# Kernel tuning notes

Measured on AMD Instinct MI355X. Metric: run time of the kernel, lower is better.

Reference implementation:

```python
import jax, jax.numpy as jnp
import numpy as np

B, S, D_MODEL, NUM_HEADS, DFF = 4, 2048, 256, 8, 1024
DEPTH = D_MODEL // NUM_HEADS
EPS = 1e-6
LENGTH_SCALE = 1.0


def setup_inputs() -> dict:
    key = jax.random.key(0)
    ks = jax.random.split(key, 18)
    n = lambda k, shp, s=0.05: (jax.random.normal(k, shp, dtype=jnp.float32) * s)
    return {
        "x": jax.random.normal(ks[0], (B, S, D_MODEL), dtype=jnp.float32),
        "wq_w": n(ks[1], (D_MODEL, D_MODEL)), "wq_b": jnp.zeros((D_MODEL,), jnp.float32),
        "wk_w": n(ks[2], (D_MODEL, D_MODEL)), "wk_b": jnp.zeros((D_MODEL,), jnp.float32),
        "wv_w": n(ks[3], (D_MODEL, D_MODEL)), "wv_b": jnp.zeros((D_MODEL,), jnp.float32),
        "wo_w": n(ks[4], (D_MODEL, D_MODEL)), "wo_b": jnp.zeros((D_MODEL,), jnp.float32),
        "ffn1_w": n(ks[5], (D_MODEL, DFF)), "ffn1_b": jnp.zeros((DFF,), jnp.float32),
        "ffn2_w": n(ks[6], (DFF, D_MODEL)), "ffn2_b": jnp.zeros((D_MODEL,), jnp.float32),
        "ln1_g": jnp.ones((D_MODEL,), jnp.float32), "ln1_b": jnp.zeros((D_MODEL,), jnp.float32),
        "ln2_g": jnp.ones((D_MODEL,), jnp.float32), "ln2_b": jnp.zeros((D_MODEL,), jnp.float32),
    }


def _layernorm(x, g, b):
    mu = jnp.mean(x, axis=-1, keepdims=True)
    var = jnp.mean(jnp.square(x - mu), axis=-1, keepdims=True)
    return (x - mu) * jax.lax.rsqrt(var + EPS) * g + b


def _split_heads(t):
    # [B,S,D_MODEL] -> [B,H,S,depth]
    return t.reshape(B, S, NUM_HEADS, DEPTH).transpose(0, 2, 1, 3)


def _encoder_layer(x, wq_w, wq_b, wk_w, wk_b, wv_w, wv_b, wo_w, wo_b,
                   ffn1_w, ffn1_b, ffn2_w, ffn2_b, ln1_g, ln1_b, ln2_g, ln2_b):
    q = _split_heads(x @ wq_w + wq_b)
    k = _split_heads(x @ wk_w + wk_b)
    v = _split_heads(x @ wv_w + wv_b)
    # pairwise squared distances: ||q||^2 - 2 q.k + ||k||^2 -> [B,H,S,S]
    q2 = jnp.sum(q * q, axis=-1)  # [B,H,S]
    k2 = jnp.sum(k * k, axis=-1)  # [B,H,S]
    dists = q2[..., :, None] - 2.0 * jnp.einsum("bhqd,bhkd->bhqk", q, k) + k2[..., None, :]
    # exponentiated-quadratic kernel, then softmax over keys (mask=None)
    attn = jax.nn.softmax(jnp.exp(-0.5 * dists / (LENGTH_SCALE ** 2)), axis=-1)
    out = jnp.einsum("bhqk,bhkd->bhqd", attn, v)  # [B,H,S,depth]
    out = out.transpose(0, 2, 1, 3).reshape(B, S, D_MODEL)
    attn_out = out @ wo_w + wo_b
    # dropout is identity (training=False)
    out1 = _layernorm(x + attn_out, ln1_g, ln1_b)
    ffn = jax.nn.relu(out1 @ ffn1_w + ffn1_b) @ ffn2_w + ffn2_b
    return _layernorm(out1 + ffn, ln2_g, ln2_b)


def reference(x, wq_w, wq_b, wk_w, wk_b, wv_w, wv_b, wo_w, wo_b,
              ffn1_w, ffn1_b, ffn2_w, ffn2_b, ln1_g, ln1_b, ln2_g, ln2_b):
    return _encoder_layer(x, wq_w, wq_b, wk_w, wk_b, wv_w, wv_b, wo_w, wo_b,
                          ffn1_w, ffn1_b, ffn2_w, ffn2_b, ln1_g, ln1_b, ln2_g, ln2_b)
```

## Files before the change

### kernel.cpp

```cpp
#include <hip/hip_runtime.h>
#include <hip/hip_bf16.h>

#define SQL  2048
#define DM   256
#define LNEPS 1e-6f
#define LOG2E    (1.44269504f)

#define B_XB    (0ull)
#define B_QB    (4ull<<20)
#define B_KB    (8ull<<20)
#define B_VT    (12ull<<20)
#define B_CTX   (16ull<<20)
#define B_O1B   (20ull<<20)
#define B_O1F   (24ull<<20)
#define B_MID   (32ull<<20)
#define B_WQKVT (48ull<<20)
#define B_WOT   ((48ull<<20)+(512ull<<10))
#define B_W1T   (49ull<<20)
#define B_W2T   ((49ull<<20)+(512ull<<10))
#define B_BQKV  (50ull<<20)
#define B_HQ    ((50ull<<20)+(64ull<<10))
#define B_HK    ((50ull<<20)+(320ull<<10))
#define B_C2    (0ull)

typedef float  f32x16 __attribute__((ext_vector_type(16)));
typedef short  bf16x8 __attribute__((ext_vector_type(8)));
typedef int    i32x4  __attribute__((ext_vector_type(4)));
typedef int    i32x2  __attribute__((ext_vector_type(2)));

static __device__ __forceinline__ unsigned short bfu(float f){
    __hip_bfloat16 h = __float2bfloat16(f);
    return *reinterpret_cast<unsigned short*>(&h);
}
static __device__ __forceinline__ unsigned pk2(float a, float b){
    return (unsigned)bfu(a) | ((unsigned)bfu(b) << 16);
}
static __device__ __forceinline__ void glds16(const void* g, void* l){
    __builtin_amdgcn_global_load_lds((const __attribute__((address_space(1))) unsigned int*)g,
                                     (__attribute__((address_space(3))) unsigned int*)l, 16, 0, 0);
}

__global__ __launch_bounds__(256) void k_packall(
    const float* __restrict__ wq, const float* __restrict__ wk, const float* __restrict__ wv,
    const float* __restrict__ wo, const float* __restrict__ w1, const float* __restrict__ w2,
    const float* __restrict__ bq, const float* __restrict__ bk, const float* __restrict__ bv,
    const float* __restrict__ x,
    unsigned short* __restrict__ wqkvT, unsigned short* __restrict__ woT,
    unsigned short* __restrict__ w1T, unsigned short* __restrict__ w2T,
    float* __restrict__ bqkv, unsigned short* __restrict__ xb)
{
    __shared__ float tile[32][33];
    const int bid = blockIdx.x;
    const int t = threadIdx.x;
    if (bid < 768) {
        const float* W; unsigned short* Wt; int K, N, xk, yn;
        if (bid < 192) {
            int which = bid >> 6, local = bid & 63;
            W = (which == 0) ? wq : (which == 1 ? wk : wv);
            Wt = wqkvT + which * 65536; K = 256; N = 256;
            xk = local & 7; yn = local >> 3;
        } else if (bid < 256) {
            int local = bid - 192; W = wo; Wt = woT; K = 256; N = 256;
            xk = local & 7; yn = local >> 3;
        } else if (bid < 512) {
            int local = bid - 256; W = w1; Wt = w1T; K = 256; N = 1024;
            xk = local & 7; yn = local >> 3;
        } else {
            int local = bid - 512; W = w2; Wt = w2T; K = 1024; N = 256;
            xk = local & 31; yn = local >> 5;
        }
        const int tx = t & 31, ty = t >> 5;
        const int kb = xk * 32, nb = yn * 32;
#pragma unroll
        for (int i = 0; i < 32; i += 8) tile[ty + i][tx] = W[(size_t)(kb + ty + i) * N + nb + tx];
        __syncthreads();
#pragma unroll
        for (int i = 0; i < 32; i += 8) Wt[(size_t)(nb + ty + i) * K + kb + tx] = bfu(tile[tx][ty + i]);
    } else if (bid < 771) {
        int wb = bid - 768;
        const float* s = (wb == 0) ? bq : (wb == 1 ? bk : bv);
        bqkv[wb * 256 + t] = s[t];
    } else {
        const int i = (bid - 771) * 256 + t;
        float4 v = ((const float4*)x)[i];
        ushort4 o; o.x = bfu(v.x); o.y = bfu(v.y); o.z = bfu(v.z); o.w = bfu(v.w);
        ((ushort4*)xb)[i] = o;
    }
}

__global__ __launch_bounds__(256, 2) void k_qkv(
    const unsigned short* __restrict__ A, const unsigned short* __restrict__ Bt,
    const float* __restrict__ bias,
    unsigned short* __restrict__ qb, unsigned short* __restrict__ kb,
    char* __restrict__ vtg)
{
    __shared__ __align__(16) char smem[65536];
    const int t = threadIdx.x;
    const int lane = t & 63, w = t >> 6;
    const int lo = lane & 31, hi = lane >> 5;
    const int row0 = blockIdx.x * 128;
    const int col0 = blockIdx.y * 128;
    f32x16 acc[2][2] = {};
    const int gS = lane & 7;
    const int rr = w * 32 + (lane >> 3);

    auto stage = [&](int buf, int kt) {
        const int k0 = kt * 64;
        char* As = smem + buf * 32768;
        char* Bs = As + 16384;
#pragma unroll
        for (int i = 0; i < 4; ++i) {
            const int r = rr + i * 8;
            glds16((const char*)(A  + (size_t)(row0 + r) * 256 + k0) + ((gS ^ (r & 7)) << 4),
                   As + w * 4096 + i * 1024 + lane * 16);
            glds16((const char*)(Bt + (size_t)(col0 + r) * 256 + k0) + ((gS ^ (r & 7)) << 4),
                   Bs + w * 4096 + i * 1024 + lane * 16);
        }
    };

    stage(0, 0);
    __syncthreads();
    for (int kt = 0; kt < 4; ++kt) {
        if (kt + 1 < 4) stage((kt + 1) & 1, kt + 1);
        const char* As = smem + (kt & 1) * 32768;
        const char* Bs = As + 16384;
        const int rA = (w >> 1) * 64 + lo;
        const int rB = (w & 1) * 64 + lo;
#pragma unroll
        for (int s = 0; s < 4; ++s) {
            const int g = s * 2 + hi;
            bf16x8 fa0 = *(const bf16x8*)(As + rA * 128 + ((g ^ (rA & 7)) << 4));
            bf16x8 fa1 = *(const bf16x8*)(As + (rA + 32) * 128 + ((g ^ (rA & 7)) << 4));
            bf16x8 fb0 = *(const bf16x8*)(Bs + rB * 128 + ((g ^ (rB & 7)) << 4));
            bf16x8 fb1 = *(const bf16x8*)(Bs + (rB + 32) * 128 + ((g ^ (rB & 7)) << 4));
            acc[0][0] = __builtin_amdgcn_mfma_f32_32x32x16_bf16(fa0, fb0, acc[0][0], 0, 0, 0);
            acc[0][1] = __builtin_amdgcn_mfma_f32_32x32x16_bf16(fa0, fb1, acc[0][1], 0, 0, 0);
            acc[1][0] = __builtin_amdgcn_mfma_f32_32x32x16_bf16(fa1, fb0, acc[1][0], 0, 0, 0);
            acc[1][1] = __builtin_amdgcn_mfma_f32_32x32x16_bf16(fa1, fb1, acc[1][1], 0, 0, 0);
        }
        __syncthreads();
    }
#pragma unroll
    for (int m = 0; m < 2; ++m)
#pragma unroll
    for (int n = 0; n < 2; ++n) {
        const int c0 = col0 + (w & 1) * 64 + n * 32;
        const int which = c0 >> 8, h = (c0 >> 5) & 7;
        const float bv = bias[c0 + lo];
        if (which < 2) {
            unsigned short* dst = (which == 0) ? qb : kb;
            const float scl = (which == 0) ? LOG2E : 1.0f;
#pragma unroll
            for (int r = 0; r < 16; ++r) {
                const int gr = row0 + (w >> 1) * 64 + m * 32 + (r & 3) + 8 * (r >> 2) + 4 * hi;
                const int b = gr >> 11, s = gr & 2047;
                dst[(((size_t)(b * 8 + h)) * SQL + s) * 32 + lo] = bfu((acc[m][n][r] + bv) * scl);
            }
        } else {
#pragma unroll
            for (int r = 0; r < 16; ++r) {
                const int gr = row0 + (w >> 1) * 64 + m * 32 + (r & 3) + 8 * (r >> 2) + 4 * hi;
                const int b = gr >> 11, s = gr & 2047;
                const int o = s * 2;
                const int op = (o & ~0x78) | ((((o >> 3) & 15) ^ (lo & 15)) << 3);
                *(unsigned short*)(vtg + ((size_t)(b * 8 + h)) * 131072 + (size_t)lo * 4096 + op)
                    = bfu(acc[m][n][r] + bv);
            }
        }
    }
}

__global__ __launch_bounds__(256) void k_h2(const unsigned short* __restrict__ qb,
                                            const unsigned short* __restrict__ kb,
                                            float* __restrict__ hq, float* __restrict__ hk)
{
    const int gid = blockIdx.x * 256 + threadIdx.x;
    const unsigned short* qp = qb + (size_t)gid * 32;
    const unsigned short* kp = kb + (size_t)gid * 32;
    float sq = 0.f, sk = 0.f;
#pragma unroll
    for (int i = 0; i < 4; ++i) {
        i32x4 qv = *(const i32x4*)(qp + i * 8);
        i32x4 kv = *(const i32x4*)(kp + i * 8);
#pragma unroll
        for (int j = 0; j < 4; ++j) {
            unsigned int qw = (unsigned int)qv[j], kw = (unsigned int)kv[j];
            float a = __builtin_bit_cast(float, qw << 16);
            float c = __builtin_bit_cast(float, qw & 0xffff0000u);
            float d = __builtin_bit_cast(float, kw << 16);
            float e = __builtin_bit_cast(float, kw & 0xffff0000u);
            sq += a * a + c * c; sk += d * d + e * e;
        }
    }
    hq[gid] = -0.34657359f * sq + 0.52876637f;
    hk[gid] = -0.72134752f * sk;
}

__global__ __launch_bounds__(512, 4) void k_attn(
    const unsigned short* __restrict__ qg, const unsigned short* __restrict__ kg,
    const char* __restrict__ vtg, const float* __restrict__ hq,
    const float* __restrict__ hk, unsigned short* __restrict__ ctxb)
{
    __shared__ __align__(16) char kls[16384];
    __shared__ __align__(16) char vtl[16384];
    __shared__ __align__(16) float hks[256];
    __shared__ __align__(16) float redacc[3 * 16 * 128];
    __shared__ __align__(16) float redden[3 * 128];
    __shared__ __align__(16) float invs[64];

    const int t = threadIdx.x;
    const int grp = t >> 7;
    const int tl  = t & 127;
    const int lane = t & 63;
    const int w   = (t >> 6) & 1;
    const int lo = lane & 31;
    const int hi = lane >> 5;

    const int bid = blockIdx.x;
    const int qc = bid & 31;
    const int bh = bid >> 5;

    const int qrow = qc * 64 + w * 32 + lo;
    const unsigned short* qp = qg + ((size_t)bh * SQL + qrow) * 32;
    bf16x8 qf0 = *(const bf16x8*)(qp + hi * 8);
    bf16x8 qf1 = *(const bf16x8*)(qp + 16 + hi * 8);
    const float hqv = hq[(size_t)bh * SQL + qrow];

    i32x4 b3i = {};
    if (hi == 0) b3i[0] = 0x3F80u | ((unsigned)bfu(hqv) << 16);
    const bf16x8 b3 = __builtin_bit_cast(bf16x8, b3i);

    f32x16 acc = {};
    float den = 0.f;

    const unsigned short* kbg = kg + (size_t)bh * SQL * 32;
    const char* vtb = vtg + (size_t)bh * 131072;
    char* kd = kls + grp * 4096;
    char* vd = vtl + grp * 4096;

    for (int kt = 0; kt < 8; ++kt) {
        const int key0 = grp * 512 + kt * 64;
        {
#pragma unroll
            for (int it = 0; it < 2; ++it) {
                const int idx = it * 128 + tl;
                const int r = idx >> 2, gl = idx & 3;
                glds16((const char*)(kbg + (size_t)(key0 + r) * 32) + ((gl ^ ((r >> 1) & 3)) << 4),
                       kd + idx * 16);
                const int vrw = idx >> 3, vch = idx & 7;
                glds16(vtb + (size_t)vrw * 4096 + key0 * 2 + vch * 16, vd + idx * 16);
            }
            if (tl < 64) hks[grp * 64 + tl] = hk[(size_t)bh * SQL + key0 + tl];
        }
        __syncthreads();

#pragma unroll
        for (int h2 = 0; h2 < 2; ++h2) {
            const int kb32 = h2 * 32;
            const int kA = kb32 + lo;
            const char* krow = kd + kA * 64;
            const int ksw = (kA >> 1) & 3;
            bf16x8 kf0 = *(const bf16x8*)(krow + (((0 + hi) ^ ksw) << 4));
            bf16x8 kf1 = *(const bf16x8*)(krow + (((2 + hi) ^ ksw) << 4));
            i32x4 a3i = {};
            if (hi == 0) a3i[0] = (unsigned)bfu(hks[grp * 64 + kA]) | 0x3F800000u;
            f32x16 sc = {};
            sc = __builtin_amdgcn_mfma_f32_32x32x16_bf16(kf0, qf0, sc, 0, 0, 0);
            sc = __builtin_amdgcn_mfma_f32_32x32x16_bf16(kf1, qf1, sc, 0, 0, 0);
            sc = __builtin_amdgcn_mfma_f32_32x32x16_bf16(
                     __builtin_bit_cast(bf16x8, a3i), b3, sc, 0, 0, 0);
            float wv[16];
#pragma unroll
            for (int r = 0; r < 16; ++r) {
                float e1 = __builtin_amdgcn_exp2f(sc[r]);
                float ww = __builtin_amdgcn_exp2f(e1);
                den += ww;
                wv[r] = ww;
            }
            i32x4 p0; p0[0]=pk2(wv[0],wv[1]);   p0[1]=pk2(wv[2],wv[3]);
                      p0[2]=pk2(wv[4],wv[5]);   p0[3]=pk2(wv[6],wv[7]);
            i32x4 p1; p1[0]=pk2(wv[8],wv[9]);   p1[1]=pk2(wv[10],wv[11]);
                      p1[2]=pk2(wv[12],wv[13]); p1[3]=pk2(wv[14],wv[15]);
            const char* vrow = vd + lo * 128;
            const int vxor = (lo & 15) << 3;
            const int o0 = (kb32 + 4 * hi) * 2;
            const int o1 = (kb32 + 16 + 4 * hi) * 2;
            i32x2 a0 = *(const i32x2*)(vrow + (o0 ^ vxor));
            i32x2 a1 = *(const i32x2*)(vrow + ((o0 + 16) ^ vxor));
            i32x2 b0 = *(const i32x2*)(vrow + (o1 ^ vxor));
            i32x2 b1 = *(const i32x2*)(vrow + ((o1 + 16) ^ vxor));
            i32x4 vb0; vb0[0]=a0[0]; vb0[1]=a0[1]; vb0[2]=a1[0]; vb0[3]=a1[1];
            i32x4 vb1; vb1[0]=b0[0]; vb1[1]=b0[1]; vb1[2]=b1[0]; vb1[3]=b1[1];
            acc = __builtin_amdgcn_mfma_f32_32x32x16_bf16(
                __builtin_bit_cast(bf16x8, p0), __builtin_bit_cast(bf16x8, vb0), acc, 0, 0, 0);
            acc = __builtin_amdgcn_mfma_f32_32x32x16_bf16(
                __builtin_bit_cast(bf16x8, p1), __builtin_bit_cast(bf16x8, vb1), acc, 0, 0, 0);
        }
        __syncthreads();
    }

    if (grp != 0) {
#pragma unroll
        for (int r = 0; r < 16; ++r) redacc[((grp - 1) * 16 + r) * 128 + tl] = acc[r];
        redden[(grp - 1) * 128 + tl] = den;
    }
    __syncthreads();
    if (grp == 0) {
#pragma unroll
        for (int r = 0; r < 16; ++r)
            acc[r] += redacc[r * 128 + tl] + redacc[(16 + r) * 128 + tl] + redacc[(32 + r) * 128 + tl];
        den += redden[tl] + redden[128 + tl] + redden[256 + tl];
        const float dfull = den + __shfl_xor(den, 32);
        if (hi == 0) invs[w * 32 + lo] = 1.f / dfull;
        float4 i0 = *(const float4*)&invs[w * 32 + 4 * hi];
        float4 i1 = *(const float4*)&invs[w * 32 + 8 + 4 * hi];
        float4 i2 = *(const float4*)&invs[w * 32 + 16 + 4 * hi];
        float4 i3 = *(const float4*)&invs[w * 32 + 24 + 4 * hi];
        float iv[16] = {i0.x,i0.y,i0.z,i0.w, i1.x,i1.y,i1.z,i1.w,
                        i2.x,i2.y,i2.z,i2.w, i3.x,i3.y,i3.z,i3.w};
        const int b = bh >> 3, h = bh & 7;
        unsigned short* cbase = ctxb + ((size_t)(b * SQL + qc * 64 + w * 32)) * 256 + h * 32 + lo;
#pragma unroll
        for (int r = 0; r < 16; ++r) {
            const int qr = (r & 3) + 8 * (r >> 2) + 4 * hi;
            cbase[(size_t)qr * 256] = bfu(acc[r] * iv[r]);
        }
    }
}

template<int KSTRIDE, int KT, int NFULL, int RELU, int OUTF, int OUTB>
__global__ __launch_bounds__(256, 2) void k_gemm(
    const unsigned short* __restrict__ A, const unsigned short* __restrict__ Bt,
    const float* __restrict__ bias,
    float* __restrict__ outf, unsigned short* __restrict__ outb)
{
    __shared__ __align__(16) char smem[65536];
    const int t = threadIdx.x;
    const int lane = t & 63, w = t >> 6;
    const int lo = lane & 31, hi = lane >> 5;
    const int row0 = blockIdx.x * 128;
    const int col0 = blockIdx.y * 128;
    const int z = blockIdx.z;
    f32x16 acc[2][2] = {};
    const int gS = lane & 7;
    const int rr = w * 32 + (lane >> 3);

    auto stage = [&](int buf, int kt) {
        const int k0 = (z * KT + kt) * 64;
        char* As = smem + buf * 32768;
        char* Bs = As + 16384;
#pragma unroll
        for (int i = 0; i < 4; ++i) {
            const int r = rr + i * 8;
            glds16((const char*)(A  + (size_t)(row0 + r) * KSTRIDE + k0) + ((gS ^ (r & 7)) << 4),
                   As + w * 4096 + i * 1024 + lane * 16);
            glds16((const char*)(Bt + (size_t)(col0 + r) * KSTRIDE + k0) + ((gS ^ (r & 7)) << 4),
                   Bs + w * 4096 + i * 1024 + lane * 16);
        }
    };

    stage(0, 0);
    __syncthreads();
    for (int kt = 0; kt < KT; ++kt) {
        if (kt + 1 < KT) stage((kt + 1) & 1, kt + 1);
        const char* As = smem + (kt & 1) * 32768;
        const char* Bs = As + 16384;
        const int rA = (w >> 1) * 64 + lo;
        const int rB = (w & 1) * 64 + lo;
#pragma unroll
        for (int s = 0; s < 4; ++s) {
            const int g = s * 2 + hi;
            bf16x8 fa0 = *(const bf16x8*)(As + rA * 128 + ((g ^ (rA & 7)) << 4));
            bf16x8 fa1 = *(const bf16x8*)(As + (rA + 32) * 128 + ((g ^ (rA & 7)) << 4));
            bf16x8 fb0 = *(const bf16x8*)(Bs + rB * 128 + ((g ^ (rB & 7)) << 4));
            bf16x8 fb1 = *(const bf16x8*)(Bs + (rB + 32) * 128 + ((g ^ (rB & 7)) << 4));
            acc[0][0] = __builtin_amdgcn_mfma_f32_32x32x16_bf16(fa0, fb0, acc[0][0], 0, 0, 0);
            acc[0][1] = __builtin_amdgcn_mfma_f32_32x32x16_bf16(fa0, fb1, acc[0][1], 0, 0, 0);
            acc[1][0] = __builtin_amdgcn_mfma_f32_32x32x16_bf16(fa1, fb0, acc[1][0], 0, 0, 0);
            acc[1][1] = __builtin_amdgcn_mfma_f32_32x32x16_bf16(fa1, fb1, acc[1][1], 0, 0, 0);
        }
        __syncthreads();
    }
#pragma unroll
    for (int m = 0; m < 2; ++m)
#pragma unroll
    for (int n = 0; n < 2; ++n) {
        const int c0 = col0 + (w & 1) * 64 + n * 32;
        const float bv = (z == 0) ? bias[c0 + lo] : 0.f;
#pragma unroll
        for (int r = 0; r < 16; ++r) {
            const int gr = row0 + (w >> 1) * 64 + m * 32 + (r & 3) + 8 * (r >> 2) + 4 * hi;
            float vv = acc[m][n][r] + bv;
            if (RELU) vv = fmaxf(vv, 0.f);
            if (OUTF) outf[(size_t)z * 8192 * NFULL + (size_t)gr * NFULL + c0 + lo] = vv;
            if (OUTB) outb[(size_t)gr * NFULL + c0 + lo] = bfu(vv);
        }
    }
}

template<int DUAL>
__global__ __launch_bounds__(256) void k_lnsum(
    const float* __restrict__ pa, const float* __restrict__ pb,
    const float* __restrict__ res, const float* __restrict__ g,
    const float* __restrict__ bt, float* __restrict__ outf,
    unsigned short* __restrict__ outb)
{
    const int row = blockIdx.x * 4 + (threadIdx.x >> 6);
    const int lane = threadIdx.x & 63;
    const size_t base = (size_t)row * 256;
    float4 v  = ((const float4*)(pa + base))[lane];
    float4 v2 = ((const float4*)(pb + base))[lane];
    float4 v3 = ((const float4*)(res + base))[lane];
    v.x += v2.x + v3.x; v.y += v2.y + v3.y; v.z += v2.z + v3.z; v.w += v2.w + v3.w;
    float s  = v.x + v.y + v.z + v.w;
    float ss = v.x * v.x + v.y * v.y + v.z * v.z + v.w * v.w;
#pragma unroll
    for (int off = 32; off; off >>= 1) { s += __shfl_xor(s, off); ss += __shfl_xor(ss, off); }
    const float mu = s * (1.f / 256.f);
    const float rstd = rsqrtf(ss * (1.f / 256.f) - mu * mu + LNEPS);
    const float4 gg = ((const float4*)g)[lane];
    const float4 bb = ((const float4*)bt)[lane];
    float4 o;
    o.x = (v.x - mu) * rstd * gg.x + bb.x;
    o.y = (v.y - mu) * rstd * gg.y + bb.y;
    o.z = (v.z - mu) * rstd * gg.z + bb.z;
    o.w = (v.w - mu) * rstd * gg.w + bb.w;
    ((float4*)(outf + base))[lane] = o;
    if (DUAL) {
        ushort4 ob; ob.x = bfu(o.x); ob.y = bfu(o.y); ob.z = bfu(o.z); ob.w = bfu(o.w);
        ((ushort4*)(outb + base))[lane] = ob;
    }
}

extern "C" void kernel_launch(void* const* d_in, const int* in_sizes, int n_in,
                              void* d_out, int out_size, void* d_ws, size_t ws_size,
                              hipStream_t stream) {
    const float* x   = (const float*)d_in[0];
    const float* wq  = (const float*)d_in[1];  const float* bq  = (const float*)d_in[2];
    const float* wk  = (const float*)d_in[3];  const float* bk  = (const float*)d_in[4];
    const float* wv  = (const float*)d_in[5];  const float* bv  = (const float*)d_in[6];
    const float* wo  = (const float*)d_in[7];  const float* wob = (const float*)d_in[8];
    const float* w1  = (const float*)d_in[9];  const float* b1  = (const float*)d_in[10];
    const float* w2  = (const float*)d_in[11]; const float* b2  = (const float*)d_in[12];
    const float* g1  = (const float*)d_in[13]; const float* bl1 = (const float*)d_in[14];
    const float* g2  = (const float*)d_in[15]; const float* bl2 = (const float*)d_in[16];

    char* ws = (char*)d_ws;
    unsigned short* xb    = (unsigned short*)(ws + B_XB);
    unsigned short* qb    = (unsigned short*)(ws + B_QB);
    unsigned short* kbuf  = (unsigned short*)(ws + B_KB);
    char*           vt    = (char*)(ws + B_VT);
    unsigned short* ctxb  = (unsigned short*)(ws + B_CTX);
    unsigned short* o1b   = (unsigned short*)(ws + B_O1B);
    float*          o1f   = (float*)(ws + B_O1F);
    unsigned short* mid   = (unsigned short*)(ws + B_MID);
    float*          c1    = (float*)(ws + B_MID);
    float*          c2    = (float*)(ws + B_C2);
    unsigned short* wqkvT = (unsigned short*)(ws + B_WQKVT);
    unsigned short* woT   = (unsigned short*)(ws + B_WOT);
    unsigned short* w1T   = (unsigned short*)(ws + B_W1T);
    unsigned short* w2T   = (unsigned short*)(ws + B_W2T);
    float* bqkv = (float*)(ws + B_BQKV);
    float* hqb  = (float*)(ws + B_HQ);
    float* hkb  = (float*)(ws + B_HK);
    float* out  = (float*)d_out;

    k_packall<<<dim3(2819), dim3(256), 0, stream>>>(wq, wk, wv, wo, w1, w2, bq, bk, bv, x,
                                                    wqkvT, woT, w1T, w2T, bqkv, xb);
    k_qkv<<<dim3(64, 6), dim3(256), 0, stream>>>(xb, wqkvT, bqkv, qb, kbuf, vt);
    k_h2<<<dim3(256), dim3(256), 0, stream>>>(qb, kbuf, hqb, hkb);
    k_attn<<<dim3(1024), dim3(512), 0, stream>>>(qb, kbuf, vt, hqb, hkb, ctxb);
    k_gemm<256, 2, 256, 0, 1, 0><<<dim3(64, 2, 2), dim3(256), 0, stream>>>(ctxb, woT, wob, c1, nullptr);
    k_lnsum<1><<<dim3(2048), dim3(256), 0, stream>>>(c1, c1 + 2097152, x, g1, bl1, o1f, o1b);
    k_gemm<256, 4, 1024, 1, 0, 1><<<dim3(64, 8, 1), dim3(256), 0, stream>>>(o1b, w1T, b1, nullptr, mid);
    k_gemm<1024, 8, 256, 0, 1, 0><<<dim3(64, 2, 2), dim3(256), 0, stream>>>(mid, w2T, b2, c2, nullptr);
    k_lnsum<0><<<dim3(2048), dim3(256), 0, stream>>>(c2, c2 + 2097152, o1f, g2, bl2, out, nullptr);
}
```

Before: 195.3 us.

## Load attention K/V fragments directly from global into registers with double buffering

The attention kernel no longer stages K and V^T tiles through LDS with per-tile __syncthreads. Each lane now loads its MFMA fragments straight from global memory into registers, double-buffered one 32-key step ahead. To support this, V^T is stored unswizzled in a plain [bh][d][s] layout, keys are loaded with a row permutation so P lines up with V without shuffles, and k_h2 writes the packed bf16 norm operands precomputed. This removes LDS traffic and block barriers, but each wave now issues uncoalesced-ish 16-byte global loads, relies on L2 for reuse across the four key groups, and uses more registers.

```diff
diff --git a/kernel.cpp b/kernel.cpp
--- a/kernel.cpp
+++ b/kernel.cpp
@@ -92,7 +92,7 @@
     const unsigned short* __restrict__ A, const unsigned short* __restrict__ Bt,
     const float* __restrict__ bias,
     unsigned short* __restrict__ qb, unsigned short* __restrict__ kb,
-    char* __restrict__ vtg)
+    unsigned short* __restrict__ vtg)
 {
     __shared__ __align__(16) char smem[65536];
     const int t = threadIdx.x;
@@ -161,10 +161,7 @@
             for (int r = 0; r < 16; ++r) {
                 const int gr = row0 + (w >> 1) * 64 + m * 32 + (r & 3) + 8 * (r >> 2) + 4 * hi;
                 const int b = gr >> 11, s = gr & 2047;
-                const int o = s * 2;
-                const int op = (o & ~0x78) | ((((o >> 3) & 15) ^ (lo & 15)) << 3);
-                *(unsigned short*)(vtg + ((size_t)(b * 8 + h)) * 131072 + (size_t)lo * 4096 + op)
-                    = bfu(acc[m][n][r] + bv);
+                vtg[((size_t)(b * 8 + h)) * 65536 + (size_t)lo * 2048 + s] = bfu(acc[m][n][r] + bv);
             }
         }
     }
@@ -172,7 +169,8 @@
 
 __global__ __launch_bounds__(256) void k_h2(const unsigned short* __restrict__ qb,
                                             const unsigned short* __restrict__ kb,
-                                            float* __restrict__ hq, float* __restrict__ hk)
+                                            unsigned int* __restrict__ hqp,
+                                            unsigned int* __restrict__ hkp)
 {
     const int gid = blockIdx.x * 256 + threadIdx.x;
     const unsigned short* qp = qb + (size_t)gid * 32;
@@ -192,18 +190,17 @@
             sq += a * a + c * c; sk += d * d + e * e;
         }
     }
-    hq[gid] = -0.34657359f * sq + 0.52876637f;
-    hk[gid] = -0.72134752f * sk;
+    const float hq = -0.34657359f * sq + 0.52876637f;
+    const float hk = -0.72134752f * sk;
+    hqp[gid] = 0x3F80u | ((unsigned)bfu(hq) << 16);
+    hkp[gid] = (unsigned)bfu(hk) | 0x3F800000u;
 }
 
 __global__ __launch_bounds__(512, 4) void k_attn(
     const unsigned short* __restrict__ qg, const unsigned short* __restrict__ kg,
-    const char* __restrict__ vtg, const float* __restrict__ hq,
-    const float* __restrict__ hk, unsigned short* __restrict__ ctxb)
-{
-    __shared__ __align__(16) char kls[16384];
-    __shared__ __align__(16) char vtl[16384];
-    __shared__ __align__(16) float hks[256];
+    const unsigned short* __restrict__ vtg, const unsigned int* __restrict__ hqp,
+    const unsigned int* __restrict__ hkp, unsigned short* __restrict__ ctxb)
+{
     __shared__ __align__(16) float redacc[3 * 16 * 128];
     __shared__ __align__(16) float redden[3 * 128];
     __shared__ __align__(16) float invs[64];
@@ -222,82 +219,69 @@
 
     const int qrow = qc * 64 + w * 32 + lo;
     const unsigned short* qp = qg + ((size_t)bh * SQL + qrow) * 32;
-    bf16x8 qf0 = *(const bf16x8*)(qp + hi * 8);
-    bf16x8 qf1 = *(const bf16x8*)(qp + 16 + hi * 8);
-    const float hqv = hq[(size_t)bh * SQL + qrow];
-
+    const bf16x8 qf0 = *(const bf16x8*)(qp + hi * 8);
+    const bf16x8 qf1 = *(const bf16x8*)(qp + 16 + hi * 8);
     i32x4 b3i = {};
-    if (hi == 0) b3i[0] = 0x3F80u | ((unsigned)bfu(hqv) << 16);
+    if (hi == 0) b3i[0] = (int)hqp[(size_t)bh * SQL + qrow];
     const bf16x8 b3 = __builtin_bit_cast(bf16x8, b3i);
+
+    const int plo = (lo & 19) | ((lo & 4) << 1) | ((lo & 8) >> 1);
+    const unsigned short* kbase = kg + (size_t)bh * SQL * 32;
+    const unsigned short* vbase = vtg + (size_t)bh * 65536 + (size_t)lo * 2048;
+    const unsigned int*   hkb   = hkp + (size_t)bh * SQL;
 
     f32x16 acc = {};
     float den = 0.f;
 
-    const unsigned short* kbg = kg + (size_t)bh * SQL * 32;
-    const char* vtb = vtg + (size_t)bh * 131072;
-    char* kd = kls + grp * 4096;
-    char* vd = vtl + grp * 4096;
-
-    for (int kt = 0; kt < 8; ++kt) {
-        const int key0 = grp * 512 + kt * 64;
-        {
-#pragma unroll
-            for (int it = 0; it < 2; ++it) {
-                const int idx = it * 128 + tl;
-                const int r = idx >> 2, gl = idx & 3;
-                glds16((const char*)(kbg + (size_t)(key0 + r) * 32) + ((gl ^ ((r >> 1) & 3)) << 4),
-                       kd + idx * 16);
-                const int vrw = idx >> 3, vch = idx & 7;
-                glds16(vtb + (size_t)vrw * 4096 + key0 * 2 + vch * 16, vd + idx * 16);
-            }
-            if (tl < 64) hks[grp * 64 + tl] = hk[(size_t)bh * SQL + key0 + tl];
-        }
-        __syncthreads();
-
-#pragma unroll
-        for (int h2 = 0; h2 < 2; ++h2) {
-            const int kb32 = h2 * 32;
-            const int kA = kb32 + lo;
-            const char* krow = kd + kA * 64;
-            const int ksw = (kA >> 1) & 3;
-            bf16x8 kf0 = *(const bf16x8*)(krow + (((0 + hi) ^ ksw) << 4));
-            bf16x8 kf1 = *(const bf16x8*)(krow + (((2 + hi) ^ ksw) << 4));
-            i32x4 a3i = {};
-            if (hi == 0) a3i[0] = (unsigned)bfu(hks[grp * 64 + kA]) | 0x3F800000u;
-            f32x16 sc = {};
-            sc = __builtin_amdgcn_mfma_f32_32x32x16_bf16(kf0, qf0, sc, 0, 0, 0);
-            sc = __builtin_amdgcn_mfma_f32_32x32x16_bf16(kf1, qf1, sc, 0, 0, 0);
-            sc = __builtin_amdgcn_mfma_f32_32x32x16_bf16(
-                     __builtin_bit_cast(bf16x8, a3i), b3, sc, 0, 0, 0);
-            float wv[16];
-#pragma unroll
-            for (int r = 0; r < 16; ++r) {
-                float e1 = __builtin_amdgcn_exp2f(sc[r]);
-                float ww = __builtin_amdgcn_exp2f(e1);
-                den += ww;
-                wv[r] = ww;
-            }
-            i32x4 p0; p0[0]=pk2(wv[0],wv[1]);   p0[1]=pk2(wv[2],wv[3]);
-                      p0[2]=pk2(wv[4],wv[5]);   p0[3]=pk2(wv[6],wv[7]);
-            i32x4 p1; p1[0]=pk2(wv[8],wv[9]);   p1[1]=pk2(wv[10],wv[11]);
-                      p1[2]=pk2(wv[12],wv[13]); p1[3]=pk2(wv[14],wv[15]);
-            const char* vrow = vd + lo * 128;
-            const int vxor = (lo & 15) << 3;
-            const int o0 = (kb32 + 4 * hi) * 2;
-            const int o1 = (kb32 + 16 + 4 * hi) * 2;
-            i32x2 a0 = *(const i32x2*)(vrow + (o0 ^ vxor));
-            i32x2 a1 = *(const i32x2*)(vrow + ((o0 + 16) ^ vxor));
-            i32x2 b0 = *(const i32x2*)(vrow + (o1 ^ vxor));
-            i32x2 b1 = *(const i32x2*)(vrow + ((o1 + 16) ^ vxor));
-            i32x4 vb0; vb0[0]=a0[0]; vb0[1]=a0[1]; vb0[2]=a1[0]; vb0[3]=a1[1];
-            i32x4 vb1; vb1[0]=b0[0]; vb1[1]=b0[1]; vb1[2]=b1[0]; vb1[3]=b1[1];
-            acc = __builtin_amdgcn_mfma_f32_32x32x16_bf16(
-                __builtin_bit_cast(bf16x8, p0), __builtin_bit_cast(bf16x8, vb0), acc, 0, 0, 0);
-            acc = __builtin_amdgcn_mfma_f32_32x32x16_bf16(
-                __builtin_bit_cast(bf16x8, p1), __builtin_bit_cast(bf16x8, vb1), acc, 0, 0, 0);
-        }
-        __syncthreads();
-    }
+#define LD(s, KF0, KF1, A3, VB0, VB1)                                              \
+    {                                                                              \
+        const int kb_ = grp * 512 + (s) * 32;                                      \
+        const int gk_ = kb_ + plo;                                                 \
+        KF0 = *(const i32x4*)(kbase + (size_t)gk_ * 32 + hi * 8);                  \
+        KF1 = *(const i32x4*)(kbase + (size_t)gk_ * 32 + 16 + hi * 8);             \
+        A3 = i32x4{};                                                              \
+        if (hi == 0) A3[0] = (int)hkb[gk_];                                        \
+        VB0 = *(const i32x4*)(vbase + kb_ + 8 * hi);                               \
+        VB1 = *(const i32x4*)(vbase + kb_ + 16 + 8 * hi);                          \
+    }
+
+    i32x4 kf0a, kf1a, a3a, vb0a, vb1a;
+    i32x4 kf0b, kf1b, a3b, vb0b, vb1b;
+    LD(0, kf0a, kf1a, a3a, vb0a, vb1a);
+#pragma unroll
+    for (int s = 0; s < 16; ++s) {
+        if (s + 1 < 16) {
+            if (s & 1) { LD(s + 1, kf0a, kf1a, a3a, vb0a, vb1a); }
+            else       { LD(s + 1, kf0b, kf1b, a3b, vb0b, vb1b); }
+        }
+        const i32x4 kf0 = (s & 1) ? kf0b : kf0a;
+        const i32x4 kf1 = (s & 1) ? kf1b : kf1a;
+        const i32x4 a3  = (s & 1) ? a3b  : a3a;
+        const i32x4 vb0 = (s & 1) ? vb0b : vb0a;
+        const i32x4 vb1 = (s & 1) ? vb1b : vb1a;
+
+        f32x16 sc = {};
+        sc = __builtin_amdgcn_mfma_f32_32x32x16_bf16(__builtin_bit_cast(bf16x8, kf0), qf0, sc, 0, 0, 0);
+        sc = __builtin_amdgcn_mfma_f32_32x32x16_bf16(__builtin_bit_cast(bf16x8, kf1), qf1, sc, 0, 0, 0);
+        sc = __builtin_amdgcn_mfma_f32_32x32x16_bf16(__builtin_bit_cast(bf16x8, a3), b3, sc, 0, 0, 0);
+        float wv[16];
+#pragma unroll
+        for (int r = 0; r < 16; ++r) {
+            float e1 = __builtin_amdgcn_exp2f(sc[r]);
+            float ww = __builtin_amdgcn_exp2f(e1);
+            den += ww;
+            wv[r] = ww;
+        }
+        i32x4 p0; p0[0]=pk2(wv[0],wv[1]);   p0[1]=pk2(wv[2],wv[3]);
+                  p0[2]=pk2(wv[4],wv[5]);   p0[3]=pk2(wv[6],wv[7]);
+        i32x4 p1; p1[0]=pk2(wv[8],wv[9]);   p1[1]=pk2(wv[10],wv[11]);
+                  p1[2]=pk2(wv[12],wv[13]); p1[3]=pk2(wv[14],wv[15]);
+        acc = __builtin_amdgcn_mfma_f32_32x32x16_bf16(
+            __builtin_bit_cast(bf16x8, p0), __builtin_bit_cast(bf16x8, vb0), acc, 0, 0, 0);
+        acc = __builtin_amdgcn_mfma_f32_32x32x16_bf16(
+            __builtin_bit_cast(bf16x8, p1), __builtin_bit_cast(bf16x8, vb1), acc, 0, 0, 0);
+    }
+#undef LD
 
     if (grp != 0) {
 #pragma unroll
@@ -449,7 +433,7 @@
     unsigned short* xb    = (unsigned short*)(ws + B_XB);
     unsigned short* qb    = (unsigned short*)(ws + B_QB);
     unsigned short* kbuf  = (unsigned short*)(ws + B_KB);
-    char*           vt    = (char*)(ws + B_VT);
+    unsigned short* vt    = (unsigned short*)(ws + B_VT);
     unsigned short* ctxb  = (unsigned short*)(ws + B_CTX);
     unsigned short* o1b   = (unsigned short*)(ws + B_O1B);
     float*          o1f   = (float*)(ws + B_O1F);
@@ -461,15 +445,15 @@
     unsigned short* w1T   = (unsigned short*)(ws + B_W1T);
     unsigned short* w2T   = (unsigned short*)(ws + B_W2T);
     float* bqkv = (float*)(ws + B_BQKV);
-    float* hqb  = (float*)(ws + B_HQ);
-    float* hkb  = (float*)(ws + B_HK);
+    unsigned int* hqp = (unsigned int*)(ws + B_HQ);
+    unsigned int* hkp = (unsigned int*)(ws + B_HK);
     float* out  = (float*)d_out;
 
     k_packall<<<dim3(2819), dim3(256), 0, stream>>>(wq, wk, wv, wo, w1, w2, bq, bk, bv, x,
                                                     wqkvT, woT, w1T, w2T, bqkv, xb);
     k_qkv<<<dim3(64, 6), dim3(256), 0, stream>>>(xb, wqkvT, bqkv, qb, kbuf, vt);
-    k_h2<<<dim3(256), dim3(256), 0, stream>>>(qb, kbuf, hqb, hkb);
-    k_attn<<<dim3(1024), dim3(512), 0, stream>>>(qb, kbuf, vt, hqb, hkb, ctxb);
+    k_h2<<<dim3(256), dim3(256), 0, stream>>>(qb, kbuf, hqp, hkp);
+    k_attn<<<dim3(1024), dim3(512), 0, stream>>>(qb, kbuf, vt, hqp, hkp, ctxb);
     k_gemm<256, 2, 256, 0, 1, 0><<<dim3(64, 2, 2), dim3(256), 0, stream>>>(ctxb, woT, wob, c1, nullptr);
     k_lnsum<1><<<dim3(2048), dim3(256), 0, stream>>>(c1, c1 + 2097152, x, g1, bl1, o1f, o1b);
     k_gemm<256, 4, 1024, 1, 0, 1><<<dim3(64, 8, 1), dim3(256), 0, stream>>>(o1b, w1T, b1, nullptr, mid);
```

Result: slower. 393.3 us (+101.4%).

## Prepack norm operands, alias attention LDS, remap blocks, and prioritize MFMA waves

Applied to the files above, without the earlier changes.

k_h2 now writes the row-norm terms already packed as bf16 MFMA operand words, so the attention kernel skips the per-tile conversion. The attention kernel's shared buffers are merged into one aliased region, with the reduction scratch reusing the K/V tile space. This cuts LDS use per block, which may allow more resident blocks. Block indices are remapped so consecutive blocks spread across heads, which could change L2 locality, and s_setprio raises wave priority around the MFMA groups to help overlap with the exp work of other waves.

```diff
diff --git a/kernel.cpp b/kernel.cpp
--- a/kernel.cpp
+++ b/kernel.cpp
@@ -172,7 +172,8 @@
 
 __global__ __launch_bounds__(256) void k_h2(const unsigned short* __restrict__ qb,
                                             const unsigned short* __restrict__ kb,
-                                            float* __restrict__ hq, float* __restrict__ hk)
+                                            unsigned int* __restrict__ hqp,
+                                            unsigned int* __restrict__ hkp)
 {
     const int gid = blockIdx.x * 256 + threadIdx.x;
     const unsigned short* qp = qb + (size_t)gid * 32;
@@ -192,21 +193,24 @@
             sq += a * a + c * c; sk += d * d + e * e;
         }
     }
-    hq[gid] = -0.34657359f * sq + 0.52876637f;
-    hk[gid] = -0.72134752f * sk;
+    const float hq = -0.34657359f * sq + 0.52876637f;
+    const float hk = -0.72134752f * sk;
+    hqp[gid] = 0x3F80u | ((unsigned)bfu(hq) << 16);
+    hkp[gid] = (unsigned)bfu(hk) | 0x3F800000u;
 }
 
 __global__ __launch_bounds__(512, 4) void k_attn(
     const unsigned short* __restrict__ qg, const unsigned short* __restrict__ kg,
-    const char* __restrict__ vtg, const float* __restrict__ hq,
-    const float* __restrict__ hk, unsigned short* __restrict__ ctxb)
-{
-    __shared__ __align__(16) char kls[16384];
-    __shared__ __align__(16) char vtl[16384];
-    __shared__ __align__(16) float hks[256];
-    __shared__ __align__(16) float redacc[3 * 16 * 128];
-    __shared__ __align__(16) float redden[3 * 128];
-    __shared__ __align__(16) float invs[64];
+    const char* __restrict__ vtg, const unsigned int* __restrict__ hqp,
+    const unsigned int* __restrict__ hkp, unsigned short* __restrict__ ctxb)
+{
+    __shared__ __align__(16) char smem[34048];
+    char* kls = smem;
+    char* vtl = smem + 16384;
+    float* hks  = (float*)(smem + 32768);
+    float* invs = (float*)(smem + 33792);
+    float* redacc = (float*)smem;
+    float* redden = (float*)(smem + 24576);
 
     const int t = threadIdx.x;
     const int grp = t >> 7;
@@ -216,18 +220,16 @@
     const int lo = lane & 31;
     const int hi = lane >> 5;
 
-    const int bid = blockIdx.x;
+    const int bid = (blockIdx.x & 7) * 128 + (blockIdx.x >> 3);
     const int qc = bid & 31;
     const int bh = bid >> 5;
 
     const int qrow = qc * 64 + w * 32 + lo;
     const unsigned short* qp = qg + ((size_t)bh * SQL + qrow) * 32;
-    bf16x8 qf0 = *(const bf16x8*)(qp + hi * 8);
-    bf16x8 qf1 = *(const bf16x8*)(qp + 16 + hi * 8);
-    const float hqv = hq[(size_t)bh * SQL + qrow];
-
+    const bf16x8 qf0 = *(const bf16x8*)(qp + hi * 8);
+    const bf16x8 qf1 = *(const bf16x8*)(qp + 16 + hi * 8);
     i32x4 b3i = {};
-    if (hi == 0) b3i[0] = 0x3F80u | ((unsigned)bfu(hqv) << 16);
+    if (hi == 0) b3i[0] = (int)hqp[(size_t)bh * SQL + qrow];
     const bf16x8 b3 = __builtin_bit_cast(bf16x8, b3i);
 
     f32x16 acc = {};
@@ -235,6 +237,7 @@
 
     const unsigned short* kbg = kg + (size_t)bh * SQL * 32;
     const char* vtb = vtg + (size_t)bh * 131072;
+    const unsigned int* hkb = hkp + (size_t)bh * SQL;
     char* kd = kls + grp * 4096;
     char* vd = vtl + grp * 4096;
 
@@ -250,7 +253,7 @@
                 const int vrw = idx >> 3, vch = idx & 7;
                 glds16(vtb + (size_t)vrw * 4096 + key0 * 2 + vch * 16, vd + idx * 16);
             }
-            if (tl < 64) hks[grp * 64 + tl] = hk[(size_t)bh * SQL + key0 + tl];
+            if (tl < 64) hks[grp * 64 + tl] = __builtin_bit_cast(float, hkb[key0 + tl]);
         }
         __syncthreads();
 
@@ -263,12 +266,14 @@
             bf16x8 kf0 = *(const bf16x8*)(krow + (((0 + hi) ^ ksw) << 4));
             bf16x8 kf1 = *(const bf16x8*)(krow + (((2 + hi) ^ ksw) << 4));
             i32x4 a3i = {};
-            if (hi == 0) a3i[0] = (unsigned)bfu(hks[grp * 64 + kA]) | 0x3F800000u;
+            if (hi == 0) a3i[0] = __builtin_bit_cast(int, hks[grp * 64 + kA]);
             f32x16 sc = {};
+            __builtin_amdgcn_s_setprio(1);
             sc = __builtin_amdgcn_mfma_f32_32x32x16_bf16(kf0, qf0, sc, 0, 0, 0);
             sc = __builtin_amdgcn_mfma_f32_32x32x16_bf16(kf1, qf1, sc, 0, 0, 0);
             sc = __builtin_amdgcn_mfma_f32_32x32x16_bf16(
                      __builtin_bit_cast(bf16x8, a3i), b3, sc, 0, 0, 0);
+            __builtin_amdgcn_s_setprio(0);
             float wv[16];
 #pragma unroll
             for (int r = 0; r < 16; ++r) {
@@ -291,10 +296,12 @@
             i32x2 b1 = *(const i32x2*)(vrow + ((o1 + 16) ^ vxor));
             i32x4 vb0; vb0[0]=a0[0]; vb0[1]=a0[1]; vb0[2]=a1[0]; vb0[3]=a1[1];
             i32x4 vb1; vb1[0]=b0[0]; vb1[1]=b0[1]; vb1[2]=b1[0]; vb1[3]=b1[1];
+            __builtin_amdgcn_s_setprio(1);
             acc = __builtin_amdgcn_mfma_f32_32x32x16_bf16(
                 __builtin_bit_cast(bf16x8, p0), __builtin_bit_cast(bf16x8, vb0), acc, 0, 0, 0);
             acc = __builtin_amdgcn_mfma_f32_32x32x16_bf16(
                 __builtin_bit_cast(bf16x8, p1), __builtin_bit_cast(bf16x8, vb1), acc, 0, 0, 0);
+            __builtin_amdgcn_s_setprio(0);
         }
         __syncthreads();
     }
@@ -461,15 +468,15 @@
     unsigned short* w1T   = (unsigned short*)(ws + B_W1T);
     unsigned short* w2T   = (unsigned short*)(ws + B_W2T);
     float* bqkv = (float*)(ws + B_BQKV);
-    float* hqb  = (float*)(ws + B_HQ);
-    float* hkb  = (float*)(ws + B_HK);
+    unsigned int* hqp = (unsigned int*)(ws + B_HQ);
+    unsigned int* hkp = (unsigned int*)(ws + B_HK);
     float* out  = (float*)d_out;
 
     k_packall<<<dim3(2819), dim3(256), 0, stream>>>(wq, wk, wv, wo, w1, w2, bq, bk, bv, x,
                                                     wqkvT, woT, w1T, w2T, bqkv, xb);
     k_qkv<<<dim3(64, 6), dim3(256), 0, stream>>>(xb, wqkvT, bqkv, qb, kbuf, vt);
-    k_h2<<<dim3(256), dim3(256), 0, stream>>>(qb, kbuf, hqb, hkb);
-    k_attn<<<dim3(1024), dim3(512), 0, stream>>>(qb, kbuf, vt, hqb, hkb, ctxb);
+    k_h2<<<dim3(256), dim3(256), 0, stream>>>(qb, kbuf, hqp, hkp);
+    k_attn<<<dim3(1024), dim3(512), 0, stream>>>(qb, kbuf, vt, hqp, hkp, ctxb);
     k_gemm<256, 2, 256, 0, 1, 0><<<dim3(64, 2, 2), dim3(256), 0, stream>>>(ctxb, woT, wob, c1, nullptr);
     k_lnsum<1><<<dim3(2048), dim3(256), 0, stream>>>(c1, c1 + 2097152, x, g1, bl1, o1f, o1b);
     k_gemm<256, 4, 1024, 1, 0, 1><<<dim3(64, 8, 1), dim3(256), 0, stream>>>(o1b, w1T, b1, nullptr, mid);
```

Measured after the change: 192.0 us. No clear change (-1.7%).
